# Performance work log

Measured on AMD Instinct MI355X. Metric: run time of the kernel, lower is better.

The kernel has to match this reference:

```python
import jax, jax.numpy as jnp
import numpy as np

B, S, D = 4, 512, 256
NEG = -1e30  # finite stand-in for -inf so fully-masked row 0 stays NaN-free


def setup_inputs() -> dict:
    key = jax.random.key(0)
    ks = jax.random.split(key, 10)
    s = 0.02
    return {
        "x": jax.random.normal(ks[0], (B, S, D), dtype=jnp.float32),
        # edge_mlp: Linear(3D -> D), ReLU, Linear(D -> 1). Stored [in, out].
        "W1": jax.random.normal(ks[1], (3 * D, D), dtype=jnp.float32) * s,
        "b1": jnp.zeros((D,), dtype=jnp.float32),
        "w2": jax.random.normal(ks[2], (D, 1), dtype=jnp.float32) * s,
        "b2": jnp.zeros((1,), dtype=jnp.float32),
        "Wv": jax.random.normal(ks[3], (D, D), dtype=jnp.float32) * s,
        "bv": jnp.zeros((D,), dtype=jnp.float32),
        "Wo": jax.random.normal(ks[4], (D, D), dtype=jnp.float32) * s,
        "bo": jnp.zeros((D,), dtype=jnp.float32),
        "gamma": jnp.ones((D,), dtype=jnp.float32),
        "beta": jnp.zeros((D,), dtype=jnp.float32),
    }


def reference(x, W1, b1, w2, b2, Wv, bv, Wo, bo, gamma, beta):
    b, seq, d = x.shape
    # edge_mlp layer1 on concat([x_i, x_j, x_i - x_j]) decomposes linearly:
    # h[b,i,j,:] = x_i @ (Wa + Wc) + x_j @ (Wb - Wc) + b1
    Wa, Wb, Wc = W1[:d], W1[d:2 * d], W1[2 * d:]
    hi = jnp.einsum('bid,dh->bih', x, Wa + Wc)          # [B,S,D]
    hj = jnp.einsum('bjd,dh->bjh', x, Wb - Wc)          # [B,S,D]
    h = jax.nn.relu(hi[:, :, None, :] + hj[:, None, :, :] + b1)  # [B,S,S,D]
    scores = jnp.einsum('bijh,h->bij', h, w2[:, 0]) + b2[0]      # [B,S,S]
    # strictly-lower-triangular causal mask (j < i)
    mask = jnp.tril(jnp.ones((seq, seq), dtype=bool), k=-1)
    scores = jnp.where(mask, scores, NEG)
    attn = jax.nn.softmax(scores, axis=-1)
    # row i=0 has no valid edges (torch yields NaN there); zero it instead
    row_valid = mask.any(axis=-1)                       # [S]
    attn = attn * row_valid[None, :, None].astype(attn.dtype)
    values = jnp.einsum('bjd,de->bje', x, Wv) + bv      # [B,S,D]
    message = jnp.einsum('bij,bjd->bid', attn, values)  # [B,S,D]
    out = jnp.einsum('bid,de->bie', message, Wo) + bo
    out = x + out
    # LayerNorm over last dim, eps=1e-5, biased variance (torch default)
    mu = jnp.mean(out, axis=-1, keepdims=True)
    var = jnp.mean(jnp.square(out - mu), axis=-1, keepdims=True)
    out = (out - mu) * jax.lax.rsqrt(var + 1e-5) * gamma + beta
    return out
```

## Files before the change

kernel.cpp:

```cpp
#include <hip/hip_runtime.h>
#include <math.h>

#define D 256
#define S 512
#define M 2048

typedef __attribute__((ext_vector_type(8))) short bf16x8;
typedef __attribute__((ext_vector_type(4))) float f32x4;

__device__ inline ushort f2bf(float f) {
    union { float f; unsigned u; } v; v.f = f;
    unsigned r = v.u + 0x7FFFu + ((v.u >> 16) & 1u);
    return (ushort)(r >> 16);
}

__global__ __launch_bounds__(256) void pack_w(
    const float* __restrict__ W1, const float* __restrict__ Wv,
    const float* __restrict__ Wo, ushort* __restrict__ WAt,
    ushort* __restrict__ WBt, ushort* __restrict__ Wvt, ushort* __restrict__ Wot)
{
    const int blk = blockIdx.x, t = threadIdx.x;
    const int mat = blk >> 4;
    const int a0 = ((blk >> 2) & 3) * 64;
    const int b0 = (blk & 3) * 64;
    __shared__ ushort lt[64][72];
    const int r = t >> 4;
    const int c = (t & 15) * 4;
#pragma unroll
    for (int p = 0; p < 4; ++p) {
        const int sr = b0 + p * 16 + r;
        float4 v;
        if (mat == 0) {
            float4 wa = *(const float4*)(W1 + (size_t)sr * 256 + a0 + c);
            float4 wc = *(const float4*)(W1 + (size_t)(512 + sr) * 256 + a0 + c);
            v = make_float4(wa.x + wc.x, wa.y + wc.y, wa.z + wc.z, wa.w + wc.w);
        } else if (mat == 1) {
            float4 wb = *(const float4*)(W1 + (size_t)(256 + sr) * 256 + a0 + c);
            float4 wc = *(const float4*)(W1 + (size_t)(512 + sr) * 256 + a0 + c);
            v = make_float4(wb.x - wc.x, wb.y - wc.y, wb.z - wc.z, wb.w - wc.w);
        } else if (mat == 2) {
            v = *(const float4*)(Wv + (size_t)sr * 256 + a0 + c);
        } else {
            v = *(const float4*)(Wo + (size_t)sr * 256 + a0 + c);
        }
        lt[p * 16 + r][c + 0] = f2bf(v.x);
        lt[p * 16 + r][c + 1] = f2bf(v.y);
        lt[p * 16 + r][c + 2] = f2bf(v.z);
        lt[p * 16 + r][c + 3] = f2bf(v.w);
    }
    __syncthreads();
    ushort* dst = (mat == 0) ? WAt : (mat == 1) ? WBt : (mat == 2) ? Wvt : Wot;
#pragma unroll
    for (int p = 0; p < 4; ++p) {
        const int dr = p * 16 + r;
        ushort4 o = make_ushort4(lt[c + 0][dr], lt[c + 1][dr],
                                 lt[c + 2][dr], lt[c + 3][dr]);
        *(ushort4*)(dst + (size_t)(a0 + dr) * 256 + b0 + c) = o;
    }
}

__global__ __launch_bounds__(256) void gemm_qkv_mfma(
    const float* __restrict__ x, const ushort* __restrict__ WAt,
    const ushort* __restrict__ WBt, const ushort* __restrict__ Wvt,
    const float* __restrict__ b1, const float* __restrict__ bv,
    float* __restrict__ hi, float* __restrict__ hj, ushort* __restrict__ vals_t)
{
    const int bn = blockIdx.x, bm = blockIdx.y;
    const int n0 = bn * 64, m0 = bm * 64;
    const int region = n0 >> 8, c0 = n0 & 255;
    const ushort* Bt = (region == 0) ? WAt : (region == 1) ? WBt : Wvt;
    const int t = threadIdx.x, w = t >> 6, l = t & 63;
    const int q = l >> 4, ln = l & 15;
    const int wm = (w >> 1) * 32, wn = (w & 1) * 32;

    __shared__ ushort T[64][72];

    f32x4 acc[2][2] = {};
    for (int k0 = 0; k0 < 256; k0 += 32) {
        union { bf16x8 v; ushort s[8]; } a[2];
        bf16x8 b[2];
#pragma unroll
        for (int mt = 0; mt < 2; ++mt) {
            const float* xr = x + (size_t)(m0 + wm + mt * 16 + ln) * 256 + k0 + q * 8;
            float4 u0 = *(const float4*)xr;
            float4 u1 = *(const float4*)(xr + 4);
            a[mt].s[0] = f2bf(u0.x); a[mt].s[1] = f2bf(u0.y);
            a[mt].s[2] = f2bf(u0.z); a[mt].s[3] = f2bf(u0.w);
            a[mt].s[4] = f2bf(u1.x); a[mt].s[5] = f2bf(u1.y);
            a[mt].s[6] = f2bf(u1.z); a[mt].s[7] = f2bf(u1.w);
        }
#pragma unroll
        for (int nt = 0; nt < 2; ++nt)
            b[nt] = *(const bf16x8*)(Bt + (size_t)(c0 + wn + nt * 16 + ln) * 256 + k0 + q * 8);
#pragma unroll
        for (int mt = 0; mt < 2; ++mt)
#pragma unroll
            for (int nt = 0; nt < 2; ++nt)
                acc[mt][nt] = __builtin_amdgcn_mfma_f32_16x16x32_bf16(a[mt].v, b[nt], acc[mt][nt], 0, 0, 0);
    }

    if (region < 2) {
        float* dst = (region == 0) ? hi : hj;
#pragma unroll
        for (int nt = 0; nt < 2; ++nt) {
            const int col = c0 + wn + nt * 16 + ln;
            const float bias = (region == 0) ? b1[col] : 0.f;
#pragma unroll
            for (int mt = 0; mt < 2; ++mt)
#pragma unroll
                for (int r = 0; r < 4; ++r) {
                    const int row = m0 + wm + mt * 16 + q * 4 + r;
                    dst[(size_t)row * 256 + col] = acc[mt][nt][r] + bias;
                }
        }
    } else {
#pragma unroll
        for (int nt = 0; nt < 2; ++nt) {
            const int cl = wn + nt * 16 + ln;
            const float bias = bv[c0 + cl];
#pragma unroll
            for (int mt = 0; mt < 2; ++mt)
#pragma unroll
                for (int r = 0; r < 4; ++r)
                    T[cl][wm + mt * 16 + q * 4 + r] = f2bf(acc[mt][nt][r] + bias);
        }
        __syncthreads();
        const int bb = m0 >> 9, jloc = m0 & 511;
#pragma unroll
        for (int p = 0; p < 2; ++p) {
            const int idx = p * 256 + t;
            const int e_l = idx & 63, jc = (idx >> 6) * 8;
            *(uint4*)(vals_t + ((size_t)(bb * 256 + c0 + e_l)) * 512 + jloc + jc) =
                *(const uint4*)&T[e_l][jc];
        }
    }
}

__global__ __launch_bounds__(256) void scores64(
    const float* __restrict__ hi, const float* __restrict__ hj,
    const float* __restrict__ w2, float* __restrict__ sc)
{
    const int jt = blockIdx.x, it = blockIdx.y, bb = blockIdx.z;
    if (jt > 2 * it + 1) return;
    const int i0 = it * 64, j0 = jt * 32;
    const int t = threadIdx.x, w = t >> 6, l = t & 63;
    const int q = l >> 4, ln = l & 15;

    __shared__ __align__(16) float His[32][64];
    __shared__ __align__(16) float Sst[64][36];
    __shared__ float w2s[256];
    if (t < 64) *(float4*)&w2s[t * 4] = *(const float4*)(w2 + t * 4);

    const int si = t & 63, sh = (t >> 6) * 8;
    const float* hisrc = hi + (size_t)((bb << 9) + i0 + si) * 256 + sh;
    const int jrow = w * 8 + q * 2;
    const float* hj0 = hj + (size_t)((bb << 9) + j0 + jrow) * 256;
    const float* hj1 = hj0 + 256;

    float acc00 = 0.f, acc01 = 0.f, acc10 = 0.f, acc11 = 0.f;
    float acc20 = 0.f, acc21 = 0.f, acc30 = 0.f, acc31 = 0.f;

    for (int hc = 0; hc < 256; hc += 32) {
        float4 a0 = *(const float4*)(hisrc + hc);
        float4 a1 = *(const float4*)(hisrc + hc + 4);
        float e0[32], e1[32];
#pragma unroll
        for (int c = 0; c < 8; ++c) {
            *(float4*)&e0[c * 4] = *(const float4*)(hj0 + hc + c * 4);
            *(float4*)&e1[c * 4] = *(const float4*)(hj1 + hc + c * 4);
        }
        __syncthreads();
        His[sh + 0][si] = a0.x; His[sh + 1][si] = a0.y;
        His[sh + 2][si] = a0.z; His[sh + 3][si] = a0.w;
        His[sh + 4][si] = a1.x; His[sh + 5][si] = a1.y;
        His[sh + 6][si] = a1.z; His[sh + 7][si] = a1.w;
        __syncthreads();
#pragma unroll
        for (int h = 0; h < 32; ++h) {
            float4 a = *(const float4*)&His[h][ln * 4];
            const float wv = w2s[hc + h];
            const float f0 = e0[h], f1 = e1[h];
            acc00 += fmaxf(a.x + f0, 0.f) * wv;
            acc01 += fmaxf(a.x + f1, 0.f) * wv;
            acc10 += fmaxf(a.y + f0, 0.f) * wv;
            acc11 += fmaxf(a.y + f1, 0.f) * wv;
            acc20 += fmaxf(a.z + f0, 0.f) * wv;
            acc21 += fmaxf(a.z + f1, 0.f) * wv;
            acc30 += fmaxf(a.w + f0, 0.f) * wv;
            acc31 += fmaxf(a.w + f1, 0.f) * wv;
        }
    }

    Sst[ln * 4 + 0][jrow] = acc00;  Sst[ln * 4 + 0][jrow + 1] = acc01;
    Sst[ln * 4 + 1][jrow] = acc10;  Sst[ln * 4 + 1][jrow + 1] = acc11;
    Sst[ln * 4 + 2][jrow] = acc20;  Sst[ln * 4 + 2][jrow + 1] = acc21;
    Sst[ln * 4 + 3][jrow] = acc30;  Sst[ln * 4 + 3][jrow + 1] = acc31;
    __syncthreads();
    const int i_l = t >> 2, jc = (t & 3) * 8;
    float* dst = sc + ((size_t)bb << 18) + (size_t)(i0 + i_l) * 512 + j0 + jc;
    *(float4*)dst       = *(const float4*)&Sst[i_l][jc];
    *(float4*)(dst + 4) = *(const float4*)&Sst[i_l][jc + 4];
}

__global__ __launch_bounds__(256) void attn_norm(
    const float* __restrict__ sc, ushort* __restrict__ attn_bf)
{
    const int row = blockIdx.x;
    const int b = row >> 9, i = row & 511;
    const int t = threadIdx.x, wave = t >> 6, lane = t & 63;
    ushort* arow = attn_bf + ((size_t)(b << 9) + i) * S;

    if (i == 0) { arow[t] = 0; arow[t + 256] = 0; return; }

    const float* srow = sc + ((size_t)b << 18) + (size_t)i * S;
    __shared__ float s[S];
    __shared__ float red[8];

    float mloc = -3.0e38f;
    for (int j = t; j < i; j += 256) { float v = srow[j]; s[j] = v; mloc = fmaxf(mloc, v); }
#pragma unroll
    for (int off = 32; off; off >>= 1) mloc = fmaxf(mloc, __shfl_xor(mloc, off, 64));
    if (lane == 0) red[wave] = mloc;
    __syncthreads();
    const float mx = fmaxf(fmaxf(red[0], red[1]), fmaxf(red[2], red[3]));

    float sloc = 0.f;
    for (int j = t; j < i; j += 256) {
        float e = __expf(s[j] - mx);
        s[j] = e;
        sloc += e;
    }
#pragma unroll
    for (int off = 32; off; off >>= 1) sloc += __shfl_xor(sloc, off, 64);
    if (lane == 0) red[4 + wave] = sloc;
    __syncthreads();
    const float inv = 1.f / (red[4] + red[5] + red[6] + red[7]);

    for (int j = t; j < S; j += 256)
        arow[j] = (j < i) ? f2bf(s[j] * inv) : (ushort)0;
}

__global__ __launch_bounds__(256) void pv_mfma(
    const ushort* __restrict__ attn_bf, const ushort* __restrict__ vals_t,
    ushort* __restrict__ msg_bf)
{
    const int bn = blockIdx.x, bm = blockIdx.y, b = blockIdx.z;
    const int n0 = bn * 64, m0 = bm * 64;
    const ushort* A = attn_bf + ((size_t)b << 18);
    const ushort* V = vals_t + (size_t)(b * 256) * 512;
    const int t = threadIdx.x, w = t >> 6, l = t & 63;
    const int q = l >> 4, ln = l & 15;
    const int wm = (w >> 1) * 32, wn = (w & 1) * 32;

    f32x4 acc[2][2] = {};
    const int kmax = m0 + 64;
    for (int k0 = 0; k0 < kmax; k0 += 32) {
        bf16x8 a[2], bb[2];
#pragma unroll
        for (int mt = 0; mt < 2; ++mt)
            a[mt] = *(const bf16x8*)(A + (size_t)(m0 + wm + mt * 16 + ln) * S + k0 + q * 8);
#pragma unroll
        for (int nt = 0; nt < 2; ++nt)
            bb[nt] = *(const bf16x8*)(V + (size_t)(n0 + wn + nt * 16 + ln) * 512 + k0 + q * 8);
#pragma unroll
        for (int mt = 0; mt < 2; ++mt)
#pragma unroll
            for (int nt = 0; nt < 2; ++nt)
                acc[mt][nt] = __builtin_amdgcn_mfma_f32_16x16x32_bf16(a[mt], bb[nt], acc[mt][nt], 0, 0, 0);
    }
#pragma unroll
    for (int nt = 0; nt < 2; ++nt) {
        const int col = n0 + wn + nt * 16 + ln;
#pragma unroll
        for (int mt = 0; mt < 2; ++mt)
#pragma unroll
            for (int r = 0; r < 4; ++r) {
                const int row = (b << 9) + m0 + wm + mt * 16 + q * 4 + r;
                msg_bf[(size_t)row * 256 + col] = f2bf(acc[mt][nt][r]);
            }
    }
}

__global__ __launch_bounds__(256) void out_ln_mfma(
    const ushort* __restrict__ msg_bf, const ushort* __restrict__ Wot,
    const float* __restrict__ x, const float* __restrict__ bo,
    const float* __restrict__ gamma, const float* __restrict__ beta,
    float* __restrict__ out)
{
    const int r0 = blockIdx.x * 16;
    const int t = threadIdx.x, w = t >> 6, l = t & 63;
    const int q = l >> 4, ln = l & 15;

    __shared__ float redS[16][4], redQ[16][4];

    f32x4 acc[4] = {};
    for (int k0 = 0; k0 < 256; k0 += 32) {
        bf16x8 a = *(const bf16x8*)(msg_bf + (size_t)(r0 + ln) * 256 + k0 + q * 8);
#pragma unroll
        for (int nt = 0; nt < 4; ++nt) {
            bf16x8 bb = *(const bf16x8*)(Wot + (size_t)(w * 64 + nt * 16 + ln) * 256 + k0 + q * 8);
            acc[nt] = __builtin_amdgcn_mfma_f32_16x16x32_bf16(a, bb, acc[nt], 0, 0, 0);
        }
    }

    float sum[4] = {}, sq[4] = {};
#pragma unroll
    for (int nt = 0; nt < 4; ++nt) {
        const int col = w * 64 + nt * 16 + ln;
        const float bov = bo[col];
#pragma unroll
        for (int r = 0; r < 4; ++r) {
            const int row = r0 + q * 4 + r;
            float v = acc[nt][r] + x[(size_t)row * 256 + col] + bov;
            acc[nt][r] = v;
            sum[r] += v;
            sq[r] += v * v;
        }
    }
#pragma unroll
    for (int r = 0; r < 4; ++r) {
#pragma unroll
        for (int off = 1; off < 16; off <<= 1) {
            sum[r] += __shfl_xor(sum[r], off, 64);
            sq[r]  += __shfl_xor(sq[r],  off, 64);
        }
    }
    if (ln == 0) {
#pragma unroll
        for (int r = 0; r < 4; ++r) {
            redS[q * 4 + r][w] = sum[r];
            redQ[q * 4 + r][w] = sq[r];
        }
    }
    __syncthreads();
#pragma unroll
    for (int nt = 0; nt < 4; ++nt) {
        const int col = w * 64 + nt * 16 + ln;
        const float g = gamma[col], be = beta[col];
#pragma unroll
        for (int r = 0; r < 4; ++r) {
            const int rl = q * 4 + r;
            const float ts = redS[rl][0] + redS[rl][1] + redS[rl][2] + redS[rl][3];
            const float tq = redQ[rl][0] + redQ[rl][1] + redQ[rl][2] + redQ[rl][3];
            const float mu = ts * (1.f / 256.f);
            const float var = tq * (1.f / 256.f) - mu * mu;
            out[(size_t)(r0 + rl) * 256 + col] =
                (acc[nt][r] - mu) * rsqrtf(var + 1e-5f) * g + be;
        }
    }
}

extern "C" void kernel_launch(void* const* d_in, const int* in_sizes, int n_in,
                              void* d_out, int out_size, void* d_ws, size_t ws_size,
                              hipStream_t stream)
{
    (void)in_sizes; (void)n_in; (void)out_size; (void)ws_size;
    const float* x     = (const float*)d_in[0];
    const float* W1    = (const float*)d_in[1];
    const float* b1    = (const float*)d_in[2];
    const float* w2    = (const float*)d_in[3];
    const float* Wv    = (const float*)d_in[5];
    const float* bv    = (const float*)d_in[6];
    const float* Wo    = (const float*)d_in[7];
    const float* bo    = (const float*)d_in[8];
    const float* gamma = (const float*)d_in[9];
    const float* beta  = (const float*)d_in[10];
    float* out = (float*)d_out;

    float* ws = (float*)d_ws;
    const size_t CH = 64 * 1024;
    float*  hi      = ws;
    float*  hj      = ws + 8 * CH;
    float*  sc      = ws + 16 * CH;
    ushort* WAt     = (ushort*)(ws + 32 * CH);
    ushort* WBt     = (ushort*)(ws + 33 * CH);
    ushort* Wvt     = (ushort*)(ws + 34 * CH);
    ushort* Wot     = (ushort*)(ws + 35 * CH);
    ushort* vals_t  = (ushort*)(ws + 36 * CH);
    ushort* attn_bf = (ushort*)(ws + 40 * CH);
    ushort* msg_bf  = (ushort*)(ws + 48 * CH);

    pack_w       <<<dim3(64),        256, 0, stream>>>(W1, Wv, Wo, WAt, WBt, Wvt, Wot);
    gemm_qkv_mfma<<<dim3(12, 32),    256, 0, stream>>>(x, WAt, WBt, Wvt, b1, bv, hi, hj, vals_t);
    scores64     <<<dim3(16, 8, 4),  256, 0, stream>>>(hi, hj, w2, sc);
    attn_norm    <<<dim3(M),         256, 0, stream>>>(sc, attn_bf);
    pv_mfma      <<<dim3(4, 8, 4),   256, 0, stream>>>(attn_bf, vals_t, msg_bf);
    out_ln_mfma  <<<dim3(128),       256, 0, stream>>>(msg_bf, Wot, x, bo, gamma, beta, out);
}
```

Before: 140.1 us.

## Fuse all stages into one cooperative persistent kernel with grid syncs

Merges the six launches into a single cooperative kernel of 256 blocks that steps through pack, QKV GEMM, scores, softmax, PV and output LayerNorm, with grid-wide syncs between stages and a union of the stages' shared-memory buffers. It also replaces the one-block-per-row softmax with a wave-per-row version that handles 8 rows per block and masks the causal entries in registers. The aim is to remove per-launch overhead and idle gaps between the small kernels. The costs are fewer blocks than some stages used before (scores and QKV now loop over work units), grid-sync latency, and a fallback to separate launches if the cooperative launch fails.

```diff
diff --git a/kernel.cpp b/kernel.cpp
--- a/kernel.cpp
+++ b/kernel.cpp
@@ -1,9 +1,13 @@
 #include <hip/hip_runtime.h>
+#include <hip/hip_cooperative_groups.h>
 #include <math.h>
+
+namespace cg = cooperative_groups;
 
 #define D 256
 #define S 512
 #define M 2048
+#define CH (64 * 1024)
 
 typedef __attribute__((ext_vector_type(8))) short bf16x8;
 typedef __attribute__((ext_vector_type(4))) float f32x4;
@@ -14,16 +18,16 @@
     return (ushort)(r >> 16);
 }
 
-__global__ __launch_bounds__(256) void pack_w(
+__device__ void pack_unit(int blk,
     const float* __restrict__ W1, const float* __restrict__ Wv,
     const float* __restrict__ Wo, ushort* __restrict__ WAt,
-    ushort* __restrict__ WBt, ushort* __restrict__ Wvt, ushort* __restrict__ Wot)
-{
-    const int blk = blockIdx.x, t = threadIdx.x;
+    ushort* __restrict__ WBt, ushort* __restrict__ Wvt, ushort* __restrict__ Wot,
+    ushort (*lt)[72])
+{
+    const int t = threadIdx.x;
     const int mat = blk >> 4;
     const int a0 = ((blk >> 2) & 3) * 64;
     const int b0 = (blk & 3) * 64;
-    __shared__ ushort lt[64][72];
     const int r = t >> 4;
     const int c = (t & 15) * 4;
 #pragma unroll
@@ -57,23 +61,22 @@
                                  lt[c + 2][dr], lt[c + 3][dr]);
         *(ushort4*)(dst + (size_t)(a0 + dr) * 256 + b0 + c) = o;
     }
-}
-
-__global__ __launch_bounds__(256) void gemm_qkv_mfma(
+    __syncthreads();
+}
+
+__device__ void qkv_unit(int bn, int bm,
     const float* __restrict__ x, const ushort* __restrict__ WAt,
     const ushort* __restrict__ WBt, const ushort* __restrict__ Wvt,
     const float* __restrict__ b1, const float* __restrict__ bv,
-    float* __restrict__ hi, float* __restrict__ hj, ushort* __restrict__ vals_t)
-{
-    const int bn = blockIdx.x, bm = blockIdx.y;
+    float* __restrict__ hi, float* __restrict__ hj, ushort* __restrict__ vals_t,
+    ushort (*T)[72])
+{
     const int n0 = bn * 64, m0 = bm * 64;
     const int region = n0 >> 8, c0 = n0 & 255;
     const ushort* Bt = (region == 0) ? WAt : (region == 1) ? WBt : Wvt;
     const int t = threadIdx.x, w = t >> 6, l = t & 63;
     const int q = l >> 4, ln = l & 15;
     const int wm = (w >> 1) * 32, wn = (w & 1) * 32;
-
-    __shared__ ushort T[64][72];
 
     f32x4 acc[2][2] = {};
     for (int k0 = 0; k0 < 256; k0 += 32) {
@@ -133,26 +136,23 @@
             *(uint4*)(vals_t + ((size_t)(bb * 256 + c0 + e_l)) * 512 + jloc + jc) =
                 *(const uint4*)&T[e_l][jc];
         }
-    }
-}
-
-__global__ __launch_bounds__(256) void scores64(
+        __syncthreads();
+    }
+}
+
+__device__ void scores_unit(int jt, int it, int bb,
     const float* __restrict__ hi, const float* __restrict__ hj,
-    const float* __restrict__ w2, float* __restrict__ sc)
-{
-    const int jt = blockIdx.x, it = blockIdx.y, bb = blockIdx.z;
-    if (jt > 2 * it + 1) return;
+    const float* __restrict__ w2, float* __restrict__ sc,
+    float (*His)[64], float (*Sst)[36], float* w2s)
+{
     const int i0 = it * 64, j0 = jt * 32;
     const int t = threadIdx.x, w = t >> 6, l = t & 63;
     const int q = l >> 4, ln = l & 15;
 
-    __shared__ __align__(16) float His[32][64];
-    __shared__ __align__(16) float Sst[64][36];
-    __shared__ float w2s[256];
     if (t < 64) *(float4*)&w2s[t * 4] = *(const float4*)(w2 + t * 4);
 
-    const int si = t & 63, sh = (t >> 6) * 8;
-    const float* hisrc = hi + (size_t)((bb << 9) + i0 + si) * 256 + sh;
+    const int si = t & 63, sh_ = (t >> 6) * 8;
+    const float* hisrc = hi + (size_t)((bb << 9) + i0 + si) * 256 + sh_;
     const int jrow = w * 8 + q * 2;
     const float* hj0 = hj + (size_t)((bb << 9) + j0 + jrow) * 256;
     const float* hj1 = hj0 + 256;
@@ -170,10 +170,10 @@
             *(float4*)&e1[c * 4] = *(const float4*)(hj1 + hc + c * 4);
         }
         __syncthreads();
-        His[sh + 0][si] = a0.x; His[sh + 1][si] = a0.y;
-        His[sh + 2][si] = a0.z; His[sh + 3][si] = a0.w;
-        His[sh + 4][si] = a1.x; His[sh + 5][si] = a1.y;
-        His[sh + 6][si] = a1.z; His[sh + 7][si] = a1.w;
+        His[sh_ + 0][si] = a0.x; His[sh_ + 1][si] = a0.y;
+        His[sh_ + 2][si] = a0.z; His[sh_ + 3][si] = a0.w;
+        His[sh_ + 4][si] = a1.x; His[sh_ + 5][si] = a1.y;
+        His[sh_ + 6][si] = a1.z; His[sh_ + 7][si] = a1.w;
         __syncthreads();
 #pragma unroll
         for (int h = 0; h < 32; ++h) {
@@ -202,49 +202,51 @@
     *(float4*)(dst + 4) = *(const float4*)&Sst[i_l][jc + 4];
 }
 
-__global__ __launch_bounds__(256) void attn_norm(
-    const float* __restrict__ sc, ushort* __restrict__ attn_bf)
-{
-    const int row = blockIdx.x;
-    const int b = row >> 9, i = row & 511;
-    const int t = threadIdx.x, wave = t >> 6, lane = t & 63;
-    ushort* arow = attn_bf + ((size_t)(b << 9) + i) * S;
-
-    if (i == 0) { arow[t] = 0; arow[t + 256] = 0; return; }
-
-    const float* srow = sc + ((size_t)b << 18) + (size_t)i * S;
-    __shared__ float s[S];
-    __shared__ float red[8];
-
-    float mloc = -3.0e38f;
-    for (int j = t; j < i; j += 256) { float v = srow[j]; s[j] = v; mloc = fmaxf(mloc, v); }
-#pragma unroll
-    for (int off = 32; off; off >>= 1) mloc = fmaxf(mloc, __shfl_xor(mloc, off, 64));
-    if (lane == 0) red[wave] = mloc;
-    __syncthreads();
-    const float mx = fmaxf(fmaxf(red[0], red[1]), fmaxf(red[2], red[3]));
-
-    float sloc = 0.f;
-    for (int j = t; j < i; j += 256) {
-        float e = __expf(s[j] - mx);
-        s[j] = e;
-        sloc += e;
-    }
-#pragma unroll
-    for (int off = 32; off; off >>= 1) sloc += __shfl_xor(sloc, off, 64);
-    if (lane == 0) red[4 + wave] = sloc;
-    __syncthreads();
-    const float inv = 1.f / (red[4] + red[5] + red[6] + red[7]);
-
-    for (int j = t; j < S; j += 256)
-        arow[j] = (j < i) ? f2bf(s[j] * inv) : (ushort)0;
-}
-
-__global__ __launch_bounds__(256) void pv_mfma(
+__device__ void softmax_rows(int bid, const float* __restrict__ sc,
+                             ushort* __restrict__ attn_bf)
+{
+    const int t = threadIdx.x, w = t >> 6, l = t & 63;
+    const int j0 = l * 8;
+#pragma unroll
+    for (int s = 0; s < 2; ++s) {
+        const int row = bid * 8 + w * 2 + s;
+        const int b = row >> 9, i = row & 511;
+        const float* srow = sc + ((size_t)b << 18) + (size_t)i * S;
+        float v[8];
+        *(float4*)&v[0] = *(const float4*)(srow + j0);
+        *(float4*)&v[4] = *(const float4*)(srow + j0 + 4);
+        float mx = -3.0e38f;
+#pragma unroll
+        for (int k = 0; k < 8; ++k) {
+            v[k] = (j0 + k < i) ? v[k] : -3.0e38f;
+            mx = fmaxf(mx, v[k]);
+        }
+#pragma unroll
+        for (int off = 32; off; off >>= 1) mx = fmaxf(mx, __shfl_xor(mx, off, 64));
+        float e[8];
+        float sum = 0.f;
+#pragma unroll
+        for (int k = 0; k < 8; ++k) {
+            e[k] = __expf(v[k] - mx);
+            sum += (j0 + k < i) ? e[k] : 0.f;
+        }
+#pragma unroll
+        for (int off = 32; off; off >>= 1) sum += __shfl_xor(sum, off, 64);
+        const float inv = (i > 0) ? (1.f / sum) : 0.f;
+        ushort o[8];
+#pragma unroll
+        for (int k = 0; k < 8; ++k)
+            o[k] = (j0 + k < i) ? f2bf(e[k] * inv) : (ushort)0;
+        ushort* arow = attn_bf + (size_t)row * S;
+        *(ushort4*)(arow + j0)     = make_ushort4(o[0], o[1], o[2], o[3]);
+        *(ushort4*)(arow + j0 + 4) = make_ushort4(o[4], o[5], o[6], o[7]);
+    }
+}
+
+__device__ void pv_unit(int bn, int bm, int b,
     const ushort* __restrict__ attn_bf, const ushort* __restrict__ vals_t,
     ushort* __restrict__ msg_bf)
 {
-    const int bn = blockIdx.x, bm = blockIdx.y, b = blockIdx.z;
     const int n0 = bn * 64, m0 = bm * 64;
     const ushort* A = attn_bf + ((size_t)b << 18);
     const ushort* V = vals_t + (size_t)(b * 256) * 512;
@@ -281,17 +283,14 @@
     }
 }
 
-__global__ __launch_bounds__(256) void out_ln_mfma(
+__device__ void outln_unit(int r0,
     const ushort* __restrict__ msg_bf, const ushort* __restrict__ Wot,
     const float* __restrict__ x, const float* __restrict__ bo,
     const float* __restrict__ gamma, const float* __restrict__ beta,
-    float* __restrict__ out)
-{
-    const int r0 = blockIdx.x * 16;
+    float* __restrict__ out, float (*redS)[4], float (*redQ)[4])
+{
     const int t = threadIdx.x, w = t >> 6, l = t & 63;
     const int q = l >> 4, ln = l & 15;
-
-    __shared__ float redS[16][4], redQ[16][4];
 
     f32x4 acc[4] = {};
     for (int k0 = 0; k0 < 256; k0 += 32) {
@@ -348,6 +347,119 @@
                 (acc[nt][r] - mu) * rsqrtf(var + 1e-5f) * g + be;
         }
     }
+}
+
+union SharedU {
+    ushort lt[64][72];
+    struct { float His[32][64]; float Sst[64][36]; float w2s[256]; } s2;
+    struct { float redS[16][4]; float redQ[16][4]; } s5;
+};
+
+__global__ __launch_bounds__(256) void fused_all(
+    const float* __restrict__ x, const float* __restrict__ W1,
+    const float* __restrict__ b1, const float* __restrict__ w2,
+    const float* __restrict__ Wv, const float* __restrict__ bv,
+    const float* __restrict__ Wo, const float* __restrict__ bo,
+    const float* __restrict__ gamma, const float* __restrict__ beta,
+    float* __restrict__ out, float* __restrict__ ws)
+{
+    float*  hi      = ws;
+    float*  hj      = ws + 8 * (size_t)CH;
+    float*  sc      = ws + 16 * (size_t)CH;
+    ushort* WAt     = (ushort*)(ws + 32 * (size_t)CH);
+    ushort* WBt     = (ushort*)(ws + 33 * (size_t)CH);
+    ushort* Wvt     = (ushort*)(ws + 34 * (size_t)CH);
+    ushort* Wot     = (ushort*)(ws + 35 * (size_t)CH);
+    ushort* vals_t  = (ushort*)(ws + 36 * (size_t)CH);
+    ushort* attn_bf = (ushort*)(ws + 40 * (size_t)CH);
+    ushort* msg_bf  = (ushort*)(ws + 48 * (size_t)CH);
+
+    __shared__ __align__(16) SharedU sh;
+    cg::grid_group grid = cg::this_grid();
+    const int bid = blockIdx.x;
+
+    if (bid < 64)
+        pack_unit(bid, W1, Wv, Wo, WAt, WBt, Wvt, Wot, sh.lt);
+    grid.sync();
+
+    for (int u = bid; u < 384; u += 256)
+        qkv_unit(u % 12, u / 12, x, WAt, WBt, Wvt, b1, bv, hi, hj, vals_t, sh.lt);
+    grid.sync();
+
+    for (int u = bid; u < 288; u += 256) {
+        const int bb = u / 72, r = u % 72;
+        int it = 0;
+        while ((it + 1) * (it + 2) <= r) ++it;
+        const int jt = r - it * (it + 1);
+        scores_unit(jt, it, bb, hi, hj, w2, sc, sh.s2.His, sh.s2.Sst, sh.s2.w2s);
+    }
+    grid.sync();
+
+    softmax_rows(bid, sc, attn_bf);
+    grid.sync();
+
+    if (bid < 128)
+        pv_unit(bid & 3, (bid >> 2) & 7, bid >> 5, attn_bf, vals_t, msg_bf);
+    grid.sync();
+
+    if (bid < 128)
+        outln_unit(bid * 16, msg_bf, Wot, x, bo, gamma, beta, out,
+                   sh.s5.redS, sh.s5.redQ);
+}
+
+__global__ __launch_bounds__(256) void pack_w_k(
+    const float* __restrict__ W1, const float* __restrict__ Wv,
+    const float* __restrict__ Wo, ushort* __restrict__ WAt,
+    ushort* __restrict__ WBt, ushort* __restrict__ Wvt, ushort* __restrict__ Wot)
+{
+    __shared__ ushort lt[64][72];
+    pack_unit(blockIdx.x, W1, Wv, Wo, WAt, WBt, Wvt, Wot, lt);
+}
+
+__global__ __launch_bounds__(256) void gemm_qkv_k(
+    const float* __restrict__ x, const ushort* __restrict__ WAt,
+    const ushort* __restrict__ WBt, const ushort* __restrict__ Wvt,
+    const float* __restrict__ b1, const float* __restrict__ bv,
+    float* __restrict__ hi, float* __restrict__ hj, ushort* __restrict__ vals_t)
+{
+    __shared__ ushort T[64][72];
+    qkv_unit(blockIdx.x, blockIdx.y, x, WAt, WBt, Wvt, b1, bv, hi, hj, vals_t, T);
+}
+
+__global__ __launch_bounds__(256) void scores_k(
+    const float* __restrict__ hi, const float* __restrict__ hj,
+    const float* __restrict__ w2, float* __restrict__ sc)
+{
+    const int jt = blockIdx.x, it = blockIdx.y, bb = blockIdx.z;
+    if (jt > 2 * it + 1) return;
+    __shared__ __align__(16) float His[32][64];
+    __shared__ __align__(16) float Sst[64][36];
+    __shared__ float w2s[256];
+    scores_unit(jt, it, bb, hi, hj, w2, sc, His, Sst, w2s);
+}
+
+__global__ __launch_bounds__(256) void softmax_k(
+    const float* __restrict__ sc, ushort* __restrict__ attn_bf)
+{
+    softmax_rows(blockIdx.x, sc, attn_bf);
+}
+
+__global__ __launch_bounds__(256) void pv_k(
+    const ushort* __restrict__ attn_bf, const ushort* __restrict__ vals_t,
+    ushort* __restrict__ msg_bf)
+{
+    pv_unit(blockIdx.x, blockIdx.y, blockIdx.z, attn_bf, vals_t, msg_bf);
+}
+
+__global__ __launch_bounds__(256) void outln_k(
+    const ushort* __restrict__ msg_bf, const ushort* __restrict__ Wot,
+    const float* __restrict__ x, const float* __restrict__ bo,
+    const float* __restrict__ gamma, const float* __restrict__ beta,
+    float* __restrict__ out)
+{
+    __shared__ float redS[16][4];
+    __shared__ float redQ[16][4];
+    outln_unit(blockIdx.x * 16, msg_bf, Wot, x, bo, gamma, beta, out, redS, redQ);
 }
 
 extern "C" void kernel_launch(void* const* d_in, const int* in_sizes, int n_in,
@@ -366,24 +478,36 @@
     const float* gamma = (const float*)d_in[9];
     const float* beta  = (const float*)d_in[10];
     float* out = (float*)d_out;
-
-    float* ws = (float*)d_ws;
-    const size_t CH = 64 * 1024;
+    float* ws  = (float*)d_ws;
+
+    static int coop_ok = -1;
+    if (coop_ok != 0) {
+        void* kargs[] = { (void*)&x, (void*)&W1, (void*)&b1, (void*)&w2,
+                          (void*)&Wv, (void*)&bv, (void*)&Wo, (void*)&bo,
+                          (void*)&gamma, (void*)&beta, (void*)&out, (void*)&ws };
+        hipError_t e = hipLaunchCooperativeKernel((const void*)fused_all,
+                                                  dim3(256), dim3(256),
+                                                  kargs, 0, stream);
+        if (e == hipSuccess) { coop_ok = 1; return; }
+        coop_ok = 0;
+        (void)hipGetLastError();
+    }
+
     float*  hi      = ws;
-    float*  hj      = ws + 8 * CH;
-    float*  sc      = ws + 16 * CH;
-    ushort* WAt     = (ushort*)(ws + 32 * CH);
-    ushort* WBt     = (ushort*)(ws + 33 * CH);
-    ushort* Wvt     = (ushort*)(ws + 34 * CH);
-    ushort* Wot     = (ushort*)(ws + 35 * CH);
-    ushort* vals_t  = (ushort*)(ws + 36 * CH);
-    ushort* attn_bf = (ushort*)(ws + 40 * CH);
-    ushort* msg_bf  = (ushort*)(ws + 48 * CH);
-
-    pack_w       <<<dim3(64),        256, 0, stream>>>(W1, Wv, Wo, WAt, WBt, Wvt, Wot);
-    gemm_qkv_mfma<<<dim3(12, 32),    256, 0, stream>>>(x, WAt, WBt, Wvt, b1, bv, hi, hj, vals_t);
-    scores64     <<<dim3(16, 8, 4),  256, 0, stream>>>(hi, hj, w2, sc);
-    attn_norm    <<<dim3(M),         256, 0, stream>>>(sc, attn_bf);
-    pv_mfma      <<<dim3(4, 8, 4),   256, 0, stream>>>(attn_bf, vals_t, msg_bf);
-    out_ln_mfma  <<<dim3(128),       256, 0, stream>>>(msg_bf, Wot, x, bo, gamma, beta, out);
-}
+    float*  hj      = ws + 8 * (size_t)CH;
+    float*  sc      = ws + 16 * (size_t)CH;
+    ushort* WAt     = (ushort*)(ws + 32 * (size_t)CH);
+    ushort* WBt     = (ushort*)(ws + 33 * (size_t)CH);
+    ushort* Wvt     = (ushort*)(ws + 34 * (size_t)CH);
+    ushort* Wot     = (ushort*)(ws + 35 * (size_t)CH);
+    ushort* vals_t  = (ushort*)(ws + 36 * (size_t)CH);
+    ushort* attn_bf = (ushort*)(ws + 40 * (size_t)CH);
+    ushort* msg_bf  = (ushort*)(ws + 48 * (size_t)CH);
+
+    pack_w_k  <<<dim3(64),       256, 0, stream>>>(W1, Wv, Wo, WAt, WBt, Wvt, Wot);
+    gemm_qkv_k<<<dim3(12, 32),   256, 0, stream>>>(x, WAt, WBt, Wvt, b1, bv, hi, hj, vals_t);
+    scores_k  <<<dim3(16, 8, 4), 256, 0, stream>>>(hi, hj, w2, sc);
+    softmax_k <<<dim3(256),      256, 0, stream>>>(sc, attn_bf);
+    pv_k      <<<dim3(4, 8, 4),  256, 0, stream>>>(attn_bf, vals_t, msg_bf);
+    outln_k   <<<dim3(128),      256, 0, stream>>>(msg_bf, Wot, x, bo, gamma, beta, out);
+}
```

Result: slower. 164.2 us (+17.1%).

## Fuse weight packing into QKV GEMM and softmax, PV, out-proj into one kernel

Applied to the files above, without the earlier changes.

The pipeline shrinks from six launches to three. Weight packing and transposition now happen inside the QKV GEMM blocks, each block staging its weight slice in shared memory, and the Wo packing runs as extra blocks in the same grid. Softmax, the attention-value product and the output projection with LayerNorm are merged into one kernel that keeps the attention and message tiles in shared memory, so the bf16 attn and msg intermediates no longer go through global memory. In exchange, each GEMM block repacks weights redundantly, and the fused tail has only 128 blocks running serial softmax and matmul phases.

```diff
diff --git a/kernel.cpp b/kernel.cpp
--- a/kernel.cpp
+++ b/kernel.cpp
@@ -4,6 +4,7 @@
 #define D 256
 #define S 512
 #define M 2048
+#define CH (64 * 1024)
 
 typedef __attribute__((ext_vector_type(8))) short bf16x8;
 typedef __attribute__((ext_vector_type(4))) float f32x4;
@@ -14,66 +15,80 @@
     return (ushort)(r >> 16);
 }
 
-__global__ __launch_bounds__(256) void pack_w(
-    const float* __restrict__ W1, const float* __restrict__ Wv,
-    const float* __restrict__ Wo, ushort* __restrict__ WAt,
-    ushort* __restrict__ WBt, ushort* __restrict__ Wvt, ushort* __restrict__ Wot)
+__global__ __launch_bounds__(256) void qkv_pack_k(
+    const float* __restrict__ x, const float* __restrict__ W1,
+    const float* __restrict__ Wv, const float* __restrict__ Wo,
+    const float* __restrict__ b1, const float* __restrict__ bv,
+    float* __restrict__ hi, float* __restrict__ hj,
+    ushort* __restrict__ vals_t, ushort* __restrict__ Wot)
 {
-    const int blk = blockIdx.x, t = threadIdx.x;
-    const int mat = blk >> 4;
-    const int a0 = ((blk >> 2) & 3) * 64;
-    const int b0 = (blk & 3) * 64;
-    __shared__ ushort lt[64][72];
-    const int r = t >> 4;
-    const int c = (t & 15) * 4;
-#pragma unroll
-    for (int p = 0; p < 4; ++p) {
-        const int sr = b0 + p * 16 + r;
-        float4 v;
-        if (mat == 0) {
-            float4 wa = *(const float4*)(W1 + (size_t)sr * 256 + a0 + c);
-            float4 wc = *(const float4*)(W1 + (size_t)(512 + sr) * 256 + a0 + c);
-            v = make_float4(wa.x + wc.x, wa.y + wc.y, wa.z + wc.z, wa.w + wc.w);
-        } else if (mat == 1) {
-            float4 wb = *(const float4*)(W1 + (size_t)(256 + sr) * 256 + a0 + c);
-            float4 wc = *(const float4*)(W1 + (size_t)(512 + sr) * 256 + a0 + c);
-            v = make_float4(wb.x - wc.x, wb.y - wc.y, wb.z - wc.z, wb.w - wc.w);
-        } else if (mat == 2) {
-            v = *(const float4*)(Wv + (size_t)sr * 256 + a0 + c);
-        } else {
-            v = *(const float4*)(Wo + (size_t)sr * 256 + a0 + c);
-        }
-        lt[p * 16 + r][c + 0] = f2bf(v.x);
-        lt[p * 16 + r][c + 1] = f2bf(v.y);
-        lt[p * 16 + r][c + 2] = f2bf(v.z);
-        lt[p * 16 + r][c + 3] = f2bf(v.w);
-    }
-    __syncthreads();
-    ushort* dst = (mat == 0) ? WAt : (mat == 1) ? WBt : (mat == 2) ? Wvt : Wot;
-#pragma unroll
-    for (int p = 0; p < 4; ++p) {
-        const int dr = p * 16 + r;
-        ushort4 o = make_ushort4(lt[c + 0][dr], lt[c + 1][dr],
-                                 lt[c + 2][dr], lt[c + 3][dr]);
-        *(ushort4*)(dst + (size_t)(a0 + dr) * 256 + b0 + c) = o;
-    }
-}
-
-__global__ __launch_bounds__(256) void gemm_qkv_mfma(
-    const float* __restrict__ x, const ushort* __restrict__ WAt,
-    const ushort* __restrict__ WBt, const ushort* __restrict__ Wvt,
-    const float* __restrict__ b1, const float* __restrict__ bv,
-    float* __restrict__ hi, float* __restrict__ hj, ushort* __restrict__ vals_t)
-{
-    const int bn = blockIdx.x, bm = blockIdx.y;
+    __shared__ union {
+        ushort Bs[64][264];
+        ushort lt[64][72];
+    } sh;
+
+    const int u = blockIdx.x;
+    const int t = threadIdx.x;
+
+    if (u >= 384) {
+        const int unit = u - 384;
+        const int a0 = (unit >> 2) * 64;
+        const int b0 = (unit & 3) * 64;
+        const int r = t >> 4;
+        const int c = (t & 15) * 4;
+#pragma unroll
+        for (int p = 0; p < 4; ++p) {
+            const int sr = b0 + p * 16 + r;
+            float4 v = *(const float4*)(Wo + (size_t)sr * 256 + a0 + c);
+            sh.lt[p * 16 + r][c + 0] = f2bf(v.x);
+            sh.lt[p * 16 + r][c + 1] = f2bf(v.y);
+            sh.lt[p * 16 + r][c + 2] = f2bf(v.z);
+            sh.lt[p * 16 + r][c + 3] = f2bf(v.w);
+        }
+        __syncthreads();
+#pragma unroll
+        for (int p = 0; p < 4; ++p) {
+            const int dr = p * 16 + r;
+            ushort4 o = make_ushort4(sh.lt[c + 0][dr], sh.lt[c + 1][dr],
+                                     sh.lt[c + 2][dr], sh.lt[c + 3][dr]);
+            *(ushort4*)(Wot + (size_t)(a0 + dr) * 256 + b0 + c) = o;
+        }
+        return;
+    }
+
+    const int bn = u % 12, bm = u / 12;
     const int n0 = bn * 64, m0 = bm * 64;
     const int region = n0 >> 8, c0 = n0 & 255;
-    const ushort* Bt = (region == 0) ? WAt : (region == 1) ? WBt : Wvt;
-    const int t = threadIdx.x, w = t >> 6, l = t & 63;
+
+    {
+        const int cl4 = (t & 15) * 4;
+        const int kb = (t >> 4) * 16;
+#pragma unroll
+        for (int kk = 0; kk < 16; ++kk) {
+            const int k = kb + kk;
+            float4 v;
+            if (region == 0) {
+                float4 wa = *(const float4*)(W1 + (size_t)k * 256 + c0 + cl4);
+                float4 wc = *(const float4*)(W1 + (size_t)(512 + k) * 256 + c0 + cl4);
+                v = make_float4(wa.x + wc.x, wa.y + wc.y, wa.z + wc.z, wa.w + wc.w);
+            } else if (region == 1) {
+                float4 wb = *(const float4*)(W1 + (size_t)(256 + k) * 256 + c0 + cl4);
+                float4 wc = *(const float4*)(W1 + (size_t)(512 + k) * 256 + c0 + cl4);
+                v = make_float4(wb.x - wc.x, wb.y - wc.y, wb.z - wc.z, wb.w - wc.w);
+            } else {
+                v = *(const float4*)(Wv + (size_t)k * 256 + c0 + cl4);
+            }
+            sh.Bs[cl4 + 0][k] = f2bf(v.x);
+            sh.Bs[cl4 + 1][k] = f2bf(v.y);
+            sh.Bs[cl4 + 2][k] = f2bf(v.z);
+            sh.Bs[cl4 + 3][k] = f2bf(v.w);
+        }
+    }
+    __syncthreads();
+
+    const int w = t >> 6, l = t & 63;
     const int q = l >> 4, ln = l & 15;
     const int wm = (w >> 1) * 32, wn = (w & 1) * 32;
-
-    __shared__ ushort T[64][72];
 
     f32x4 acc[2][2] = {};
     for (int k0 = 0; k0 < 256; k0 += 32) {
@@ -91,7 +106,7 @@
         }
 #pragma unroll
         for (int nt = 0; nt < 2; ++nt)
-            b[nt] = *(const bf16x8*)(Bt + (size_t)(c0 + wn + nt * 16 + ln) * 256 + k0 + q * 8);
+            b[nt] = *(const bf16x8*)&sh.Bs[wn + nt * 16 + ln][k0 + q * 8];
 #pragma unroll
         for (int mt = 0; mt < 2; ++mt)
 #pragma unroll
@@ -114,6 +129,7 @@
                 }
         }
     } else {
+        __syncthreads();
 #pragma unroll
         for (int nt = 0; nt < 2; ++nt) {
             const int cl = wn + nt * 16 + ln;
@@ -122,7 +138,7 @@
             for (int mt = 0; mt < 2; ++mt)
 #pragma unroll
                 for (int r = 0; r < 4; ++r)
-                    T[cl][wm + mt * 16 + q * 4 + r] = f2bf(acc[mt][nt][r] + bias);
+                    sh.lt[cl][wm + mt * 16 + q * 4 + r] = f2bf(acc[mt][nt][r] + bias);
         }
         __syncthreads();
         const int bb = m0 >> 9, jloc = m0 & 511;
@@ -131,12 +147,12 @@
             const int idx = p * 256 + t;
             const int e_l = idx & 63, jc = (idx >> 6) * 8;
             *(uint4*)(vals_t + ((size_t)(bb * 256 + c0 + e_l)) * 512 + jloc + jc) =
-                *(const uint4*)&T[e_l][jc];
-        }
-    }
-}
-
-__global__ __launch_bounds__(256) void scores64(
+                *(const uint4*)&sh.lt[e_l][jc];
+        }
+    }
+}
+
+__global__ __launch_bounds__(256) void scores_k(
     const float* __restrict__ hi, const float* __restrict__ hj,
     const float* __restrict__ w2, float* __restrict__ sc)
 {
@@ -151,8 +167,8 @@
     __shared__ float w2s[256];
     if (t < 64) *(float4*)&w2s[t * 4] = *(const float4*)(w2 + t * 4);
 
-    const int si = t & 63, sh = (t >> 6) * 8;
-    const float* hisrc = hi + (size_t)((bb << 9) + i0 + si) * 256 + sh;
+    const int si = t & 63, sh_ = (t >> 6) * 8;
+    const float* hisrc = hi + (size_t)((bb << 9) + i0 + si) * 256 + sh_;
     const int jrow = w * 8 + q * 2;
     const float* hj0 = hj + (size_t)((bb << 9) + j0 + jrow) * 256;
     const float* hj1 = hj0 + 256;
@@ -170,10 +186,10 @@
             *(float4*)&e1[c * 4] = *(const float4*)(hj1 + hc + c * 4);
         }
         __syncthreads();
-        His[sh + 0][si] = a0.x; His[sh + 1][si] = a0.y;
-        His[sh + 2][si] = a0.z; His[sh + 3][si] = a0.w;
-        His[sh + 4][si] = a1.x; His[sh + 5][si] = a1.y;
-        His[sh + 6][si] = a1.z; His[sh + 7][si] = a1.w;
+        His[sh_ + 0][si] = a0.x; His[sh_ + 1][si] = a0.y;
+        His[sh_ + 2][si] = a0.z; His[sh_ + 3][si] = a0.w;
+        His[sh_ + 4][si] = a1.x; His[sh_ + 5][si] = a1.y;
+        His[sh_ + 6][si] = a1.z; His[sh_ + 7][si] = a1.w;
         __syncthreads();
 #pragma unroll
         for (int h = 0; h < 32; ++h) {
@@ -202,107 +218,88 @@
     *(float4*)(dst + 4) = *(const float4*)&Sst[i_l][jc + 4];
 }
 
-__global__ __launch_bounds__(256) void attn_norm(
-    const float* __restrict__ sc, ushort* __restrict__ attn_bf)
+__global__ __launch_bounds__(256) void smpvout_k(
+    const float* __restrict__ sc, const ushort* __restrict__ vals_t,
+    const ushort* __restrict__ Wot, const float* __restrict__ x,
+    const float* __restrict__ bo, const float* __restrict__ gamma,
+    const float* __restrict__ beta, float* __restrict__ out)
 {
-    const int row = blockIdx.x;
-    const int b = row >> 9, i = row & 511;
-    const int t = threadIdx.x, wave = t >> 6, lane = t & 63;
-    ushort* arow = attn_bf + ((size_t)(b << 9) + i) * S;
-
-    if (i == 0) { arow[t] = 0; arow[t + 256] = 0; return; }
-
-    const float* srow = sc + ((size_t)b << 18) + (size_t)i * S;
-    __shared__ float s[S];
-    __shared__ float red[8];
-
-    float mloc = -3.0e38f;
-    for (int j = t; j < i; j += 256) { float v = srow[j]; s[j] = v; mloc = fmaxf(mloc, v); }
-#pragma unroll
-    for (int off = 32; off; off >>= 1) mloc = fmaxf(mloc, __shfl_xor(mloc, off, 64));
-    if (lane == 0) red[wave] = mloc;
-    __syncthreads();
-    const float mx = fmaxf(fmaxf(red[0], red[1]), fmaxf(red[2], red[3]));
-
-    float sloc = 0.f;
-    for (int j = t; j < i; j += 256) {
-        float e = __expf(s[j] - mx);
-        s[j] = e;
-        sloc += e;
-    }
-#pragma unroll
-    for (int off = 32; off; off >>= 1) sloc += __shfl_xor(sloc, off, 64);
-    if (lane == 0) red[4 + wave] = sloc;
-    __syncthreads();
-    const float inv = 1.f / (red[4] + red[5] + red[6] + red[7]);
-
-    for (int j = t; j < S; j += 256)
-        arow[j] = (j < i) ? f2bf(s[j] * inv) : (ushort)0;
-}
-
-__global__ __launch_bounds__(256) void pv_mfma(
-    const ushort* __restrict__ attn_bf, const ushort* __restrict__ vals_t,
-    ushort* __restrict__ msg_bf)
-{
-    const int bn = blockIdx.x, bm = blockIdx.y, b = blockIdx.z;
-    const int n0 = bn * 64, m0 = bm * 64;
-    const ushort* A = attn_bf + ((size_t)b << 18);
-    const ushort* V = vals_t + (size_t)(b * 256) * 512;
+    const int u = blockIdx.x;
+    const int b = u >> 5, m0 = (u & 31) * 16;
     const int t = threadIdx.x, w = t >> 6, l = t & 63;
     const int q = l >> 4, ln = l & 15;
-    const int wm = (w >> 1) * 32, wn = (w & 1) * 32;
-
-    f32x4 acc[2][2] = {};
-    const int kmax = m0 + 64;
+
+    __shared__ __align__(16) ushort attnS[16][520];
+    __shared__ __align__(16) ushort msgS[16][264];
+    __shared__ float redS[16][4], redQ[16][4];
+
+    {
+        const int j0 = l * 8;
+#pragma unroll
+        for (int rr = 0; rr < 4; ++rr) {
+            const int rl = w * 4 + rr;
+            const int i = m0 + rl;
+            const float* srow = sc + ((size_t)b << 18) + (size_t)i * S;
+            float v[8];
+            *(float4*)&v[0] = *(const float4*)(srow + j0);
+            *(float4*)&v[4] = *(const float4*)(srow + j0 + 4);
+            float mx = -3.0e38f;
+#pragma unroll
+            for (int k = 0; k < 8; ++k) {
+                v[k] = (j0 + k < i) ? v[k] : -3.0e38f;
+                mx = fmaxf(mx, v[k]);
+            }
+#pragma unroll
+            for (int off = 32; off; off >>= 1) mx = fmaxf(mx, __shfl_xor(mx, off, 64));
+            float e[8];
+            float sum = 0.f;
+#pragma unroll
+            for (int k = 0; k < 8; ++k) {
+                e[k] = __expf(v[k] - mx);
+                sum += (j0 + k < i) ? e[k] : 0.f;
+            }
+#pragma unroll
+            for (int off = 32; off; off >>= 1) sum += __shfl_xor(sum, off, 64);
+            const float inv = (i > 0) ? (1.f / sum) : 0.f;
+            ushort o[8];
+#pragma unroll
+            for (int k = 0; k < 8; ++k)
+                o[k] = (j0 + k < i) ? f2bf(e[k] * inv) : (ushort)0;
+            *(ushort4*)&attnS[rl][j0]     = make_ushort4(o[0], o[1], o[2], o[3]);
+            *(ushort4*)&attnS[rl][j0 + 4] = make_ushort4(o[4], o[5], o[6], o[7]);
+        }
+    }
+    __syncthreads();
+
+    const ushort* V = vals_t + (size_t)b * 256 * 512;
+    f32x4 acc[4] = {};
+    const int kmax = (m0 + 16 + 31) & ~31;
     for (int k0 = 0; k0 < kmax; k0 += 32) {
-        bf16x8 a[2], bb[2];
-#pragma unroll
-        for (int mt = 0; mt < 2; ++mt)
-            a[mt] = *(const bf16x8*)(A + (size_t)(m0 + wm + mt * 16 + ln) * S + k0 + q * 8);
-#pragma unroll
-        for (int nt = 0; nt < 2; ++nt)
-            bb[nt] = *(const bf16x8*)(V + (size_t)(n0 + wn + nt * 16 + ln) * 512 + k0 + q * 8);
-#pragma unroll
-        for (int mt = 0; mt < 2; ++mt)
-#pragma unroll
-            for (int nt = 0; nt < 2; ++nt)
-                acc[mt][nt] = __builtin_amdgcn_mfma_f32_16x16x32_bf16(a[mt], bb[nt], acc[mt][nt], 0, 0, 0);
-    }
-#pragma unroll
-    for (int nt = 0; nt < 2; ++nt) {
-        const int col = n0 + wn + nt * 16 + ln;
-#pragma unroll
-        for (int mt = 0; mt < 2; ++mt)
-#pragma unroll
-            for (int r = 0; r < 4; ++r) {
-                const int row = (b << 9) + m0 + wm + mt * 16 + q * 4 + r;
-                msg_bf[(size_t)row * 256 + col] = f2bf(acc[mt][nt][r]);
-            }
-    }
-}
-
-__global__ __launch_bounds__(256) void out_ln_mfma(
-    const ushort* __restrict__ msg_bf, const ushort* __restrict__ Wot,
-    const float* __restrict__ x, const float* __restrict__ bo,
-    const float* __restrict__ gamma, const float* __restrict__ beta,
-    float* __restrict__ out)
-{
-    const int r0 = blockIdx.x * 16;
-    const int t = threadIdx.x, w = t >> 6, l = t & 63;
-    const int q = l >> 4, ln = l & 15;
-
-    __shared__ float redS[16][4], redQ[16][4];
-
-    f32x4 acc[4] = {};
+        bf16x8 a = *(const bf16x8*)&attnS[ln][k0 + q * 8];
+#pragma unroll
+        for (int nt = 0; nt < 4; ++nt) {
+            bf16x8 bb = *(const bf16x8*)(V + (size_t)(w * 64 + nt * 16 + ln) * 512 + k0 + q * 8);
+            acc[nt] = __builtin_amdgcn_mfma_f32_16x16x32_bf16(a, bb, acc[nt], 0, 0, 0);
+        }
+    }
+#pragma unroll
+    for (int nt = 0; nt < 4; ++nt)
+#pragma unroll
+        for (int r = 0; r < 4; ++r)
+            msgS[q * 4 + r][w * 64 + nt * 16 + ln] = f2bf(acc[nt][r]);
+    __syncthreads();
+
+    f32x4 acc2[4] = {};
     for (int k0 = 0; k0 < 256; k0 += 32) {
-        bf16x8 a = *(const bf16x8*)(msg_bf + (size_t)(r0 + ln) * 256 + k0 + q * 8);
+        bf16x8 a = *(const bf16x8*)&msgS[ln][k0 + q * 8];
 #pragma unroll
         for (int nt = 0; nt < 4; ++nt) {
             bf16x8 bb = *(const bf16x8*)(Wot + (size_t)(w * 64 + nt * 16 + ln) * 256 + k0 + q * 8);
-            acc[nt] = __builtin_amdgcn_mfma_f32_16x16x32_bf16(a, bb, acc[nt], 0, 0, 0);
-        }
-    }
-
+            acc2[nt] = __builtin_amdgcn_mfma_f32_16x16x32_bf16(a, bb, acc2[nt], 0, 0, 0);
+        }
+    }
+
+    const int r0 = (b << 9) + m0;
     float sum[4] = {}, sq[4] = {};
 #pragma unroll
     for (int nt = 0; nt < 4; ++nt) {
@@ -311,8 +308,8 @@
 #pragma unroll
         for (int r = 0; r < 4; ++r) {
             const int row = r0 + q * 4 + r;
-            float v = acc[nt][r] + x[(size_t)row * 256 + col] + bov;
-            acc[nt][r] = v;
+            float v = acc2[nt][r] + x[(size_t)row * 256 + col] + bov;
+            acc2[nt][r] = v;
             sum[r] += v;
             sq[r] += v * v;
         }
@@ -345,7 +342,7 @@
             const float mu = ts * (1.f / 256.f);
             const float var = tq * (1.f / 256.f) - mu * mu;
             out[(size_t)(r0 + rl) * 256 + col] =
-                (acc[nt][r] - mu) * rsqrtf(var + 1e-5f) * g + be;
+                (acc2[nt][r] - mu) * rsqrtf(var + 1e-5f) * g + be;
         }
     }
 }
@@ -368,22 +365,13 @@
     float* out = (float*)d_out;
 
     float* ws = (float*)d_ws;
-    const size_t CH = 64 * 1024;
-    float*  hi      = ws;
-    float*  hj      = ws + 8 * CH;
-    float*  sc      = ws + 16 * CH;
-    ushort* WAt     = (ushort*)(ws + 32 * CH);
-    ushort* WBt     = (ushort*)(ws + 33 * CH);
-    ushort* Wvt     = (ushort*)(ws + 34 * CH);
-    ushort* Wot     = (ushort*)(ws + 35 * CH);
-    ushort* vals_t  = (ushort*)(ws + 36 * CH);
-    ushort* attn_bf = (ushort*)(ws + 40 * CH);
-    ushort* msg_bf  = (ushort*)(ws + 48 * CH);
-
-    pack_w       <<<dim3(64),        256, 0, stream>>>(W1, Wv, Wo, WAt, WBt, Wvt, Wot);
-    gemm_qkv_mfma<<<dim3(12, 32),    256, 0, stream>>>(x, WAt, WBt, Wvt, b1, bv, hi, hj, vals_t);
-    scores64     <<<dim3(16, 8, 4),  256, 0, stream>>>(hi, hj, w2, sc);
-    attn_norm    <<<dim3(M),         256, 0, stream>>>(sc, attn_bf);
-    pv_mfma      <<<dim3(4, 8, 4),   256, 0, stream>>>(attn_bf, vals_t, msg_bf);
-    out_ln_mfma  <<<dim3(128),       256, 0, stream>>>(msg_bf, Wot, x, bo, gamma, beta, out);
-}
+    float*  hi     = ws;
+    float*  hj     = ws + 8 * (size_t)CH;
+    float*  sc     = ws + 16 * (size_t)CH;
+    ushort* Wot    = (ushort*)(ws + 32 * (size_t)CH);
+    ushort* vals_t = (ushort*)(ws + 33 * (size_t)CH);
+
+    qkv_pack_k<<<dim3(400),      256, 0, stream>>>(x, W1, Wv, Wo, b1, bv, hi, hj, vals_t, Wot);
+    scores_k  <<<dim3(16, 8, 4), 256, 0, stream>>>(hi, hj, w2, sc);
+    smpvout_k <<<dim3(128),      256, 0, stream>>>(sc, vals_t, Wot, x, bo, gamma, beta, out);
+}
```

Measured after the change: 135.1 us. -3.6%, faster.
